# Kernel optimization log

Measured on AMD Instinct MI355X. Metric: run time of the kernel, lower is better.

## Reference

```python
import jax, jax.numpy as jnp
import numpy as np

B, N, C = 8, 4096, 768
H, HD = 12, 64          # num_heads, head_dim = C // H
M = HD * 2              # rand_feat_dim
LAM = 0.3
NUM_STEP = 5


def setup_inputs() -> dict:
    key = jax.random.key(0)
    k1, k2, k3, k4 = jax.random.split(key, 4)
    x = jax.random.normal(k1, (B, N, C), dtype=jnp.float32)
    Wqkv = jax.random.normal(k2, (C, 2 * C), dtype=jnp.float32) * 0.02
    Wproj = jax.random.normal(k3, (C, C), dtype=jnp.float32) * 0.02
    bproj = jnp.zeros((C,), dtype=jnp.float32)
    rand_matrix = jax.random.normal(k4, (H, HD, M), dtype=jnp.float32)
    return {"x": x, "Wqkv": Wqkv, "Wproj": Wproj, "bproj": bproj,
            "rand_matrix": rand_matrix}


def _soft(z, t):
    # sign(z) * relu(|z| - t): soft-thresholding (ISTA proximal step)
    return jnp.sign(z) * jax.nn.relu(jnp.abs(z) - t)


def reference(x, Wqkv, Wproj, bproj, rand_matrix):
    Bn, Nn, Cn = x.shape
    Hh, hd, m = rand_matrix.shape
    scale = hd ** (-0.5)

    qkv = x @ Wqkv                                   # [B,N,2C]
    q = qkv[..., :Cn].reshape(Bn, Nn, Hh, hd).transpose(0, 2, 1, 3)  # [B,H,N,hd]
    v = qkv[..., Cn:].reshape(Bn, Nn, Hh, hd).transpose(0, 2, 1, 3)  # [B,H,N,hd]

    # random-feature map: exp(q @ proj - ||q||^2 / 2) / sqrt(m)
    qs = q * scale ** 0.5
    rf = jnp.exp(jnp.einsum('bhnd,hdm->bhnm', qs, rand_matrix)
                 - 0.5 * jnp.sum(qs * qs, axis=-1, keepdims=True)) / m ** 0.5
    # F.normalize(p=2, dim=-2): normalize over the sequence axis
    qn = rf / jnp.maximum(jnp.linalg.norm(rf, axis=-2, keepdims=True), 1e-12)

    kk = jnp.einsum('bhnm,bhnp->bhmp', qn, qn)       # [B,H,m,m]
    kv = jnp.einsum('bhnm,bhnd->bhmd', qn, v)        # [B,H,m,hd]

    # Lipschitz bound: max row L1 norm of kk, detached
    L = jax.lax.stop_gradient(
        jnp.max(jnp.sum(jnp.abs(kk), axis=-1), axis=-1))[..., None, None] + 1.0

    # unrolled ISTA soft-thresholding loop
    s = _soft(kv, LAM)
    for _ in range(NUM_STEP):
        s = _soft(s - (kk @ s - kv) / L, LAM / L)

    out = jnp.einsum('bhnm,bhmd->bhnd', qn, s)       # [B,H,N,hd]
    out = out.transpose(0, 2, 1, 3).reshape(Bn, Nn, Cn)
    return out @ Wproj + bproj
```

## Files before the change

kernel.cpp:

```cpp
#include <hip/hip_runtime.h>


typedef __attribute__((ext_vector_type(8))) short bf16x8;
typedef __attribute__((ext_vector_type(4))) float f32x4;

#define GLD16(gptr, lptr)                                                              \
  __builtin_amdgcn_global_load_lds((const __attribute__((address_space(1))) void*)(gptr), \
                                   (__attribute__((address_space(3))) void*)(lptr), 16, 0, 0)

__device__ __forceinline__ unsigned short f2bf(float f) {
  union { float f; unsigned int u; } v; v.f = f;
  unsigned int r = v.u + 0x7fffu + ((v.u >> 16) & 1u);
  return (unsigned short)(r >> 16);
}
__device__ __forceinline__ float bf2f(unsigned short s) {
  union { unsigned int u; float f; } v; v.u = ((unsigned int)s) << 16;
  return v.f;
}
__device__ __forceinline__ float rn_of(float css) {
  return 1.f / fmaxf(sqrtf(css), 1e-12f);
}

template<int ITERS>
__device__ __forceinline__ void gemm256_core(
    const unsigned short* __restrict__ A,
    const unsigned short* __restrict__ B,
    int ldk,
    f32x4 (&acc)[8][4],
    unsigned short* smem) {
  const int tid = threadIdx.x;
  const int lane = tid & 63, wave = tid >> 6;
  const int l16 = lane & 15, quad = lane >> 4;
  const int wr = wave >> 2, wc = wave & 3;
  const int rsw = l16 & 7;

#pragma unroll
  for (int i = 0; i < 8; i++)
#pragma unroll
    for (int j = 0; j < 4; j++)
#pragma unroll
      for (int r = 0; r < 4; r++) acc[i][j][r] = 0.f;

  const int srow0 = tid >> 3, sc0 = ((tid & 7) ^ (srow0 & 7)) << 3;
  const int srow1 = (tid + 512) >> 3, sc1 = ((tid & 7) ^ (srow1 & 7)) << 3;
  const int dstw = wave * 512;

  auto stageA = [&](int T, int h) {
    const unsigned short* g = A + (long)(h * 128) * ldk + T * 64;
    unsigned short* d = smem + (T & 1) * 32768 + h * 8192 + dstw;
    GLD16(g + (long)srow0 * ldk + sc0, d);
    GLD16(g + (long)srow1 * ldk + sc1, d + 4096);
  };
  auto stageB = [&](int T, int h) {
    const unsigned short* g = B + (long)(h * 128) * ldk + T * 64;
    unsigned short* d = smem + (T & 1) * 32768 + 16384 + h * 8192 + dstw;
    GLD16(g + (long)srow0 * ldk + sc0, d);
    GLD16(g + (long)srow1 * ldk + sc1, d + 4096);
  };

  bf16x8 af[4][2], bn0[2][2], bn1[2][2];

  auto rdA = [&](int b, int mh) {
    const unsigned short* p = smem + b * 32768 + wr * 8192 + (mh * 64 + l16) * 64;
#pragma unroll
    for (int ii = 0; ii < 4; ii++)
#pragma unroll
      for (int ks = 0; ks < 2; ks++)
        af[ii][ks] = *(const bf16x8*)(p + ii * 1024 + (((ks * 4 + quad) ^ rsw) << 3));
  };
  auto rdB = [&](bf16x8 (&bf)[2][2], int b, int nh) {
    const unsigned short* p = smem + b * 32768 + 16384 + (wc >> 1) * 8192 +
                              ((wc & 1) * 64 + nh * 32 + l16) * 64;
#pragma unroll
    for (int jj = 0; jj < 2; jj++)
#pragma unroll
      for (int ks = 0; ks < 2; ks++)
        bf[jj][ks] = *(const bf16x8*)(p + jj * 1024 + (((ks * 4 + quad) ^ rsw) << 3));
  };

  auto mma = [&](bf16x8 (&bf)[2][2], int mh, int nh) {
    __builtin_amdgcn_s_setprio(1);
#pragma unroll
    for (int ks = 0; ks < 2; ks++)
#pragma unroll
      for (int ii = 0; ii < 4; ii++)
#pragma unroll
        for (int jj = 0; jj < 2; jj++)
          acc[mh * 4 + ii][nh * 2 + jj] = __builtin_amdgcn_mfma_f32_16x16x32_bf16(
              af[ii][ks], bf[jj][ks], acc[mh * 4 + ii][nh * 2 + jj], 0, 0, 0);
    __builtin_amdgcn_s_setprio(0);
  };

#define FENCE asm volatile("" ::: "memory")
#define DRAIN                                             \
  asm volatile("s_waitcnt lgkmcnt(0)" ::: "memory");      \
  __builtin_amdgcn_sched_barrier(0)

  stageA(0, 0); stageA(0, 1); stageB(0, 0); stageB(0, 1);
  stageB(1, 0); stageB(1, 1);
  asm volatile("s_waitcnt vmcnt(4)" ::: "memory");
  __builtin_amdgcn_s_barrier();

#pragma unroll 1
  for (int i = 0; i < ITERS; i++) {
    const int u = 2 * i;
    const bool more = (i < ITERS - 1);
    stageA(u + 1, 0);
    rdA(0, 0); rdB(bn0, 0, 0);
    FENCE; __builtin_amdgcn_s_barrier(); DRAIN;
    mma(bn0, 0, 0);
    FENCE; __builtin_amdgcn_s_barrier();
    stageA(u + 1, 1);
    rdB(bn1, 0, 1);
    FENCE; __builtin_amdgcn_s_barrier(); DRAIN;
    mma(bn1, 0, 1);
    FENCE; __builtin_amdgcn_s_barrier();
    if (more) stageB(u + 2, 0);
    rdA(0, 1);
    FENCE; __builtin_amdgcn_s_barrier(); DRAIN;
    mma(bn1, 1, 1);
    FENCE; __builtin_amdgcn_s_barrier();
    if (more) stageB(u + 2, 1);
    FENCE; __builtin_amdgcn_s_barrier(); DRAIN;
    mma(bn0, 1, 0);
    if (more) { asm volatile("s_waitcnt vmcnt(4)" ::: "memory"); }
    else      { asm volatile("s_waitcnt vmcnt(0)" ::: "memory"); }
    FENCE; __builtin_amdgcn_s_barrier();
    if (more) stageA(u + 2, 0);
    rdA(1, 0); rdB(bn0, 1, 0);
    FENCE; __builtin_amdgcn_s_barrier(); DRAIN;
    mma(bn0, 0, 0);
    FENCE; __builtin_amdgcn_s_barrier();
    if (more) stageA(u + 2, 1);
    rdB(bn1, 1, 1);
    FENCE; __builtin_amdgcn_s_barrier(); DRAIN;
    mma(bn1, 0, 1);
    FENCE; __builtin_amdgcn_s_barrier();
    if (more) stageB(u + 3, 0);
    rdA(1, 1);
    FENCE; __builtin_amdgcn_s_barrier(); DRAIN;
    mma(bn1, 1, 1);
    FENCE; __builtin_amdgcn_s_barrier();
    if (more) stageB(u + 3, 1);
    FENCE; __builtin_amdgcn_s_barrier(); DRAIN;
    mma(bn0, 1, 0);
    asm volatile("s_waitcnt vmcnt(4)" ::: "memory");
    FENCE; __builtin_amdgcn_s_barrier();
  }
#undef FENCE
#undef DRAIN
}

template<int BM, int BN>
__device__ __forceinline__ void gemm_core_nt(
    const unsigned short* __restrict__ A, int lda,
    const unsigned short* __restrict__ B0,
    const unsigned short* __restrict__ B1, int brows0, int ldb,
    int K,
    f32x4 (&acc)[BM / 32][BN / 32],
    unsigned short* As, unsigned short* Bs) {
  constexpr int MT = BM / 32, NT = BN / 32;
  const int tid = threadIdx.x;
  const int lane = tid & 63, wave = tid >> 6;
  const int wm = (wave >> 1) * (BM / 2), wn = (wave & 1) * (BN / 2);
  const int l16 = lane & 15, quad = lane >> 4;
  const int arow = tid >> 2;
  const int akos = (((tid & 3) ^ ((arow >> 1) & 3)) << 3);
  const int fsw = (l16 >> 1) & 3;
#pragma unroll
  for (int i = 0; i < MT; i++)
#pragma unroll
    for (int j = 0; j < NT; j++)
#pragma unroll
      for (int r = 0; r < 4; r++) acc[i][j][r] = 0.f;

  for (int k0 = 0; k0 < K; k0 += 32) {
    __syncthreads();
#pragma unroll
    for (int c = 0; c < BM / 64; c++) {
      const unsigned short* gp = A + (long)(arow + c * 64) * lda + k0 + akos;
      GLD16(gp, As + (c * 256 + wave * 64) * 8);
    }
#pragma unroll
    for (int c = 0; c < BN / 64; c++) {
      int row = arow + c * 64;
      const unsigned short* bp = (row < brows0) ? (B0 + (long)row * ldb)
                                                : (B1 + (long)(row - brows0) * ldb);
      GLD16(bp + k0 + akos, Bs + (c * 256 + wave * 64) * 8);
    }
    __syncthreads();
    bf16x8 af[MT], bfr[NT];
#pragma unroll
    for (int i = 0; i < MT; i++)
      af[i] = *(const bf16x8*)(As + (wm + i * 16 + l16) * 32 + ((quad ^ fsw) * 8));
#pragma unroll
    for (int j = 0; j < NT; j++)
      bfr[j] = *(const bf16x8*)(Bs + (wn + j * 16 + l16) * 32 + ((quad ^ fsw) * 8));
#pragma unroll
    for (int i = 0; i < MT; i++)
#pragma unroll
      for (int j = 0; j < NT; j++)
        acc[i][j] = __builtin_amdgcn_mfma_f32_16x16x32_bf16(af[i], bfr[j], acc[i][j], 0, 0, 0);
  }
}

__global__ __launch_bounds__(256) void k_convert_bf16(const float* __restrict__ in,
                                                      unsigned short* __restrict__ out, long n4) {
  long i = (long)blockIdx.x * 256 + threadIdx.x;
  if (i < n4) {
    float4 v = ((const float4*)in)[i];
    unsigned short o[4] = {f2bf(v.x), f2bf(v.y), f2bf(v.z), f2bf(v.w)};
    ((uint2*)out)[i] = *(uint2*)o;
  }
}

__global__ __launch_bounds__(256) void k_transpose_tiled(const float* __restrict__ in,
                                                         unsigned short* __restrict__ out,
                                                         int R, int C, float scale) {
  __shared__ float t[32][33];
  const float* ib = in + (long)blockIdx.z * R * C;
  unsigned short* ob = out + (long)blockIdx.z * R * C;
  int c0 = blockIdx.x * 32, r0 = blockIdx.y * 32;
  int tx = threadIdx.x & 31, ty = threadIdx.x >> 5;
#pragma unroll
  for (int k = 0; k < 32; k += 8)
    t[ty + k][tx] = ib[(long)(r0 + ty + k) * C + c0 + tx];
  __syncthreads();
#pragma unroll
  for (int k = 0; k < 32; k += 8)
    ob[(long)(c0 + ty + k) * R + r0 + tx] = f2bf(t[tx][ty + k] * scale);
}

__global__ __launch_bounds__(512, 2) void k_gemm_qkv256(const unsigned short* __restrict__ xbf,
                                                        const unsigned short* __restrict__ wqkvT,
                                                        unsigned short* __restrict__ q,
                                                        unsigned short* __restrict__ vT) {
  __shared__ __align__(16) unsigned short smem[65536];
  f32x4 acc[8][4];
  const int L = blockIdx.x;
  const int xcd = L & 7, slot = L >> 3;
  const int rt = xcd * 16 + slot / 6;
  const int ct = slot % 6;
  gemm256_core<6>(xbf + (long)rt * 256 * 768, wqkvT + (long)ct * 256 * 768, 768, acc, smem);

  const int tid = threadIdx.x, lane = tid & 63, wave = tid >> 6;
  const int l16 = lane & 15, quad = lane >> 4;
  const int wr = wave >> 2, wc = wave & 3;
  const int b = rt >> 4;
  const int nbase = (rt & 15) * 256;
  if (ct < 3) {
#pragma unroll
    for (int i = 0; i < 8; i++)
#pragma unroll
      for (int j = 0; j < 4; j++) {
        int col = ct * 256 + wc * 64 + j * 16 + l16;
        int h = col >> 6, d = col & 63;
#pragma unroll
        for (int r = 0; r < 4; r++) {
          int n = nbase + wr * 128 + i * 16 + quad * 4 + r;
          q[((long)(b * 12 + h) * 4096 + n) * 64 + d] = f2bf(acc[i][j][r]);
        }
      }
  } else {
    unsigned short* pool = smem;
    for (int hh = 0; hh < 2; hh++) {
      __syncthreads();
      if (wr == hh) {
#pragma unroll
        for (int i = 0; i < 8; i++)
#pragma unroll
          for (int j = 0; j < 4; j++)
#pragma unroll
            for (int r = 0; r < 4; r++)
              pool[(wc * 64 + j * 16 + l16) * 136 + i * 16 + quad * 4 + r] = f2bf(acc[i][j][r]);
      }
      __syncthreads();
#pragma unroll
      for (int it = 0; it < 8; it++) {
        int chunk = it * 512 + tid;
        int col = chunk >> 4, ng = chunk & 15;
        uint4 val = *(const uint4*)&pool[col * 136 + ng * 8];
        int vcol = (ct - 3) * 256 + col;
        int h = vcol >> 6, d = vcol & 63;
        long n = nbase + hh * 128 + ng * 8;
        *(uint4*)&vT[((long)(b * 12 + h) * 64 + d) * 4096 + n] = val;
      }
    }
  }
}

__global__ __launch_bounds__(256) void k_gemm_rf(const unsigned short* __restrict__ q,
                                                 const unsigned short* __restrict__ rmT,
                                                 unsigned short* __restrict__ qnT,
                                                 float* __restrict__ colss) {
  __shared__ __align__(16) unsigned short smem[16384];
  __shared__ float hnp[256];
  __shared__ float css[128];
  unsigned short* Asm = smem;
  unsigned short* Bsm = smem + 8192;
  unsigned short* pool = smem;
  f32x4 acc[4][4];
  const int nt = blockIdx.x, bh = blockIdx.y, h = bh % 12;
  const int tid = threadIdx.x, lane = tid & 63, wave = tid >> 6;
  const int l16 = lane & 15, quad = lane >> 4;
  const int wm = (wave >> 1) * 64, wn = (wave & 1) * 64;
  const int fsw = (l16 >> 1) & 3;
  const unsigned short* Aq = q + ((long)bh * 4096 + nt * 128) * 64;
  const unsigned short* Brm = rmT + (long)h * 8192;

#pragma unroll
  for (int c = 0; c < 4; c++) {
    int chunk = c * 256 + tid;
    int row = chunk >> 3, ko8 = chunk & 7;
    int kc = ko8 >> 2;
    int c2s = (ko8 & 3) ^ ((row >> 1) & 3);
    *(uint4*)(Asm + kc * 4096 + row * 32 + c2s * 8) = *(const uint4*)(Aq + (long)row * 64 + ko8 * 8);
    *(uint4*)(Bsm + kc * 4096 + row * 32 + c2s * 8) = *(const uint4*)(Brm + (long)row * 64 + ko8 * 8);
  }
  for (int i = tid; i < 128; i += 256) css[i] = 0.f;
  __syncthreads();
  {
    const unsigned short* ap = Asm + (tid & 1) * 4096 + (tid >> 1) * 32;
    float ssum = 0.f;
#pragma unroll
    for (int e = 0; e < 32; e++) { float f = bf2f(ap[e]); ssum += f * f; }
    hnp[tid] = ssum;
  }
#pragma unroll
  for (int i = 0; i < 4; i++)
#pragma unroll
    for (int j = 0; j < 4; j++)
#pragma unroll
      for (int r = 0; r < 4; r++) acc[i][j][r] = 0.f;
#pragma unroll
  for (int kc = 0; kc < 2; kc++) {
    bf16x8 af[4], bfr[4];
#pragma unroll
    for (int i = 0; i < 4; i++)
      af[i] = *(const bf16x8*)(Asm + kc * 4096 + (wm + i * 16 + l16) * 32 + ((quad ^ fsw) * 8));
#pragma unroll
    for (int j = 0; j < 4; j++)
      bfr[j] = *(const bf16x8*)(Bsm + kc * 4096 + (wn + j * 16 + l16) * 32 + ((quad ^ fsw) * 8));
#pragma unroll
    for (int i = 0; i < 4; i++)
#pragma unroll
      for (int j = 0; j < 4; j++)
        acc[i][j] = __builtin_amdgcn_mfma_f32_16x16x32_bf16(af[i], bfr[j], acc[i][j], 0, 0, 0);
  }
  __syncthreads();
  float hnv[4][4];
#pragma unroll
  for (int i = 0; i < 4; i++)
#pragma unroll
    for (int r = 0; r < 4; r++) {
      int row = wm + i * 16 + quad * 4 + r;
      hnv[i][r] = 0.0625f * (hnp[2 * row] + hnp[2 * row + 1]);
    }
#pragma unroll
  for (int j = 0; j < 4; j++) {
    int col = wn + j * 16 + l16;
    float cp = 0.f;
#pragma unroll
    for (int i = 0; i < 4; i++)
#pragma unroll
      for (int r = 0; r < 4; r++) {
        float v = __expf(acc[i][j][r] - hnv[i][r]) * 0.08838834764831845f;
        acc[i][j][r] = v;
        cp += v * v;
      }
    atomicAdd(&css[col], cp);
  }
  __syncthreads();
  for (int i = tid; i < 128; i += 256) atomicAdd(&colss[bh * 128 + i], css[i]);
  for (int hh = 0; hh < 2; hh++) {
    __syncthreads();
    if ((wave >> 1) == hh) {
#pragma unroll
      for (int i = 0; i < 4; i++)
#pragma unroll
        for (int j = 0; j < 4; j++)
#pragma unroll
          for (int r = 0; r < 4; r++)
            pool[(i * 16 + quad * 4 + r) * 134 + wn + j * 16 + l16] = f2bf(acc[i][j][r]);
    }
    __syncthreads();
#pragma unroll
    for (int c = 0; c < 4; c++) {
      int chunk = tid + c * 256;
      int m = chunk >> 3, nj = (chunk & 7) * 8;
      unsigned short o[8];
#pragma unroll
      for (int e = 0; e < 8; e++) o[e] = pool[(nj + e) * 134 + m];
      *(uint4*)&qnT[((long)bh * 128 + m) * 4096 + nt * 128 + hh * 64 + nj] = *(uint4*)o;
    }
  }
}

__global__ __launch_bounds__(256) void k_gemm_kkkv(const unsigned short* __restrict__ qnT,
                                                   const unsigned short* __restrict__ vT,
                                                   const float* __restrict__ colss,
                                                   unsigned short* __restrict__ kkp) {
  __shared__ __align__(16) unsigned short As[128 * 32], Bs[192 * 32];
  f32x4 acc[4][6];
  const int ks = blockIdx.x, bh = blockIdx.y;
  const unsigned short* A = qnT + (long)bh * 128 * 4096 + ks * 512;
  const unsigned short* B1 = vT + (long)bh * 64 * 4096 + ks * 512;
  gemm_core_nt<128, 192>(A, 4096, A, B1, 128, 4096, 512, acc, As, Bs);
  const int lane = threadIdx.x & 63, wave = threadIdx.x >> 6;
  const int l16 = lane & 15, quad = lane >> 4;
  const int wm = (wave >> 1) * 64, wn = (wave & 1) * 96;
  unsigned short* dst = kkp + ((long)ks * 96 + bh) * 24576;
  float rnr[4][4];
#pragma unroll
  for (int i = 0; i < 4; i++)
#pragma unroll
    for (int r = 0; r < 4; r++)
      rnr[i][r] = rn_of(colss[bh * 128 + wm + i * 16 + quad * 4 + r]);
#pragma unroll
  for (int j = 0; j < 6; j++) {
    int col = wn + j * 16 + l16;
    float rnc = (col < 128) ? rn_of(colss[bh * 128 + col]) : 1.f;
#pragma unroll
    for (int i = 0; i < 4; i++)
#pragma unroll
      for (int r = 0; r < 4; r++) {
        int row = wm + i * 16 + quad * 4 + r;
        dst[row * 192 + col] = f2bf(acc[i][j][r] * rnr[i][r] * rnc);
      }
  }
}

__global__ __launch_bounds__(256) void k_ista(const unsigned short* __restrict__ kkp,
                                              const float* __restrict__ colss,
                                              unsigned short* __restrict__ sT) {
  __shared__ __align__(16) unsigned short kks[128 * 144];
  __shared__ __align__(16) unsigned short ssT[64 * 144];
  __shared__ float kvs[128 * 64];
  __shared__ float red[128];
  __shared__ float rns[128];
  const int tid = threadIdx.x, lane = tid & 63, wave = tid >> 6;
  const int l16 = lane & 15, quad = lane >> 4;
  const int wm = (wave >> 1) * 64, wn = (wave & 1) * 32;
  const int bh = blockIdx.x;
  const unsigned short* base = kkp + (long)bh * 24576;
  for (int idx = tid; idx < 3072; idx += 256) {
    int m = idx / 24, c8 = idx % 24;
    float f[8] = {0.f, 0.f, 0.f, 0.f, 0.f, 0.f, 0.f, 0.f};
#pragma unroll
    for (int ks = 0; ks < 8; ks++) {
      union { uint4 u; unsigned short s[8]; } u;
      u.u = *(const uint4*)(base + (long)ks * 2359296 + m * 192 + c8 * 8);
#pragma unroll
      for (int e = 0; e < 8; e++) f[e] += bf2f(u.s[e]);
    }
    if (c8 < 16) {
#pragma unroll
      for (int e = 0; e < 8; e++) kks[m * 144 + c8 * 8 + e] = f2bf(f[e]);
    } else {
#pragma unroll
      for (int e = 0; e < 8; e++) kvs[m * 64 + (c8 - 16) * 8 + e] = f[e];
    }
  }
  __syncthreads();
  float kv[4][2][4];
#pragma unroll
  for (int i = 0; i < 4; i++)
#pragma unroll
    for (int j = 0; j < 2; j++)
#pragma unroll
      for (int r = 0; r < 4; r++) {
        int m = wm + i * 16 + quad * 4 + r, d = wn + j * 16 + l16;
        kv[i][j][r] = kvs[m * 64 + d];
      }
  if (tid < 128) {
    float rs = 0.f;
    const unsigned short* rp = kks + tid * 144;
    for (int p = 0; p < 128; p++) rs += fabsf(bf2f(rp[p]));
    red[tid] = rs;
    rns[tid] = rn_of(colss[bh * 128 + tid]);
  }
  __syncthreads();
  for (int o = 64; o > 0; o >>= 1) {
    if (tid < o) red[tid] = fmaxf(red[tid], red[tid + o]);
    __syncthreads();
  }
  const float L = red[0] + 1.f;
  const float invL = 1.f / L;
  const float lamL = 0.3f * invL;
  float sreg[4][2][4];
#pragma unroll
  for (int i = 0; i < 4; i++)
#pragma unroll
    for (int j = 0; j < 2; j++)
#pragma unroll
      for (int r = 0; r < 4; r++) {
        float z = kv[i][j][r];
        float az = fabsf(z) - 0.3f;
        float s = az > 0.f ? copysignf(az, z) : 0.f;
        sreg[i][j][r] = s;
        ssT[(wn + j * 16 + l16) * 144 + wm + i * 16 + quad * 4 + r] = f2bf(s);
      }
  for (int step = 0; step < 5; step++) {
    __syncthreads();
    f32x4 acc[4][2];
#pragma unroll
    for (int i = 0; i < 4; i++)
#pragma unroll
      for (int j = 0; j < 2; j++)
#pragma unroll
        for (int r = 0; r < 4; r++) acc[i][j][r] = 0.f;
#pragma unroll
    for (int kc = 0; kc < 4; kc++) {
      bf16x8 af[4], bfj[2];
#pragma unroll
      for (int i = 0; i < 4; i++)
        af[i] = *(const bf16x8*)(kks + (wm + i * 16 + l16) * 144 + kc * 32 + quad * 8);
#pragma unroll
      for (int j = 0; j < 2; j++)
        bfj[j] = *(const bf16x8*)(ssT + (wn + j * 16 + l16) * 144 + kc * 32 + quad * 8);
#pragma unroll
      for (int i = 0; i < 4; i++)
#pragma unroll
        for (int j = 0; j < 2; j++)
          acc[i][j] = __builtin_amdgcn_mfma_f32_16x16x32_bf16(af[i], bfj[j], acc[i][j], 0, 0, 0);
    }
    __syncthreads();
#pragma unroll
    for (int i = 0; i < 4; i++)
#pragma unroll
      for (int j = 0; j < 2; j++)
#pragma unroll
        for (int r = 0; r < 4; r++) {
          float z = sreg[i][j][r] - (acc[i][j][r] - kv[i][j][r]) * invL;
          float az = fabsf(z) - lamL;
          float s = az > 0.f ? copysignf(az, z) : 0.f;
          sreg[i][j][r] = s;
          ssT[(wn + j * 16 + l16) * 144 + wm + i * 16 + quad * 4 + r] = f2bf(s);
        }
  }
#pragma unroll
  for (int i = 0; i < 4; i++)
#pragma unroll
    for (int j = 0; j < 2; j++)
#pragma unroll
      for (int r = 0; r < 4; r++) {
        int m = wm + i * 16 + quad * 4 + r, d = wn + j * 16 + l16;
        sT[(long)bh * 8192 + d * 128 + m] = f2bf(sreg[i][j][r] * rns[m]);
      }
}

__global__ __launch_bounds__(256) void k_gemm_attn(const unsigned short* __restrict__ qnT,
                                                   const unsigned short* __restrict__ sT,
                                                   unsigned short* __restrict__ attn) {
  __shared__ __align__(16) unsigned short As2[32 * 128];
  __shared__ __align__(16) unsigned short Bs[64 * 32];
  f32x4 acc[4][2];
  const int nt = blockIdx.x, bh = blockIdx.y;
  const int b = bh / 12, h = bh % 12;
  const int tid = threadIdx.x, lane = tid & 63, wave = tid >> 6;
  const int l16 = lane & 15, quad = lane >> 4;
  const int wm = (wave >> 1) * 64, wn = (wave & 1) * 32;
  const int fsw = (l16 >> 1) & 3;
#pragma unroll
  for (int i = 0; i < 4; i++)
#pragma unroll
    for (int j = 0; j < 2; j++)
#pragma unroll
      for (int r = 0; r < 4; r++) acc[i][j][r] = 0.f;
  for (int k0 = 0; k0 < 128; k0 += 32) {
    __syncthreads();
#pragma unroll
    for (int c = 0; c < 2; c++) {
      int chunk = tid + c * 256;
      int kr = chunk >> 4, n0 = (chunk & 15) * 8;
      const unsigned short* gp = qnT + ((long)bh * 128 + k0 + kr) * 4096 + nt * 128 + n0;
      GLD16(gp, As2 + (c * 256 + wave * 64) * 8);
    }
    {
      int dd = tid >> 2;
      int ko = (((tid & 3) ^ ((dd >> 1) & 3)) * 8);
      const unsigned short* gp = sT + ((long)bh * 64 + dd) * 128 + k0 + ko;
      GLD16(gp, Bs + wave * 512);
    }
    __syncthreads();
    bf16x8 af[4], bfr[2];
#pragma unroll
    for (int i = 0; i < 4; i++) {
      union { bf16x8 v; unsigned short s[8]; } u;
#pragma unroll
      for (int e = 0; e < 8; e++) u.s[e] = As2[(quad * 8 + e) * 128 + wm + i * 16 + l16];
      af[i] = u.v;
    }
#pragma unroll
    for (int j = 0; j < 2; j++)
      bfr[j] = *(const bf16x8*)&Bs[(wn + j * 16 + l16) * 32 + ((quad ^ fsw) * 8)];
#pragma unroll
    for (int i = 0; i < 4; i++)
#pragma unroll
      for (int j = 0; j < 2; j++)
        acc[i][j] = __builtin_amdgcn_mfma_f32_16x16x32_bf16(af[i], bfr[j], acc[i][j], 0, 0, 0);
  }
#pragma unroll
  for (int i = 0; i < 4; i++)
#pragma unroll
    for (int j = 0; j < 2; j++)
#pragma unroll
      for (int r = 0; r < 4; r++) {
        int n = nt * 128 + wm + i * 16 + quad * 4 + r;
        int dd = wn + j * 16 + l16;
        attn[((long)b * 4096 + n) * 768 + h * 64 + dd] = f2bf(acc[i][j][r]);
      }
}

__global__ __launch_bounds__(512, 2) void k_gemm_proj256(const unsigned short* __restrict__ attn,
                                                         const unsigned short* __restrict__ wprojT,
                                                         const float* __restrict__ bias,
                                                         float* __restrict__ out) {
  __shared__ __align__(16) unsigned short smem[65536];
  f32x4 acc[8][4];
  const int L = blockIdx.x;
  const int xcd = L & 7, slot = L >> 3;
  const int rt = xcd * 16 + slot / 3;
  const int ct = slot % 3;
  gemm256_core<6>(attn + (long)rt * 256 * 768, wprojT + (long)ct * 256 * 768, 768, acc, smem);
  const int tid = threadIdx.x, lane = tid & 63, wave = tid >> 6;
  const int l16 = lane & 15, quad = lane >> 4;
  const int wr = wave >> 2, wc = wave & 3;
  const long row0 = (long)rt * 256 + wr * 128;
#pragma unroll
  for (int i = 0; i < 8; i++)
#pragma unroll
    for (int j = 0; j < 4; j++) {
      int col = ct * 256 + wc * 64 + j * 16 + l16;
      float bv = bias[col];
#pragma unroll
      for (int r = 0; r < 4; r++) {
        long row = row0 + i * 16 + quad * 4 + r;
        out[row * 768 + col] = acc[i][j][r] + bv;
      }
    }
}

extern "C" void kernel_launch(void* const* d_in, const int* in_sizes, int n_in,
                              void* d_out, int out_size, void* d_ws, size_t ws_size,
                              hipStream_t stream) {
  const float* x = (const float*)d_in[0];
  const float* Wqkv = (const float*)d_in[1];
  const float* Wproj = (const float*)d_in[2];
  const float* bproj = (const float*)d_in[3];
  const float* rm = (const float*)d_in[4];
  float* out = (float*)d_out;

  size_t o = 0;
  char* wsb = (char*)d_ws;
  auto take = [&](size_t b) { char* p = wsb + o; o += b; return p; };
  unsigned short* wqkvT = (unsigned short*)take(2359296);
  unsigned short* wprojT = (unsigned short*)take(1179648);
  unsigned short* rmT = (unsigned short*)take(196608);
  unsigned short* q = (unsigned short*)take(50331648);
  unsigned short* vT = (unsigned short*)take(50331648);
  float* colss = (float*)take(49152);
  unsigned short* sT = (unsigned short*)take(1572864);
  if (ws_size < o) return;

  unsigned short* xbf = (unsigned short*)d_out;
  unsigned short* qnT = (unsigned short*)d_out;
  unsigned short* kkp = q;
  unsigned short* attnbf = q;

  hipMemsetAsync(colss, 0, 49152, stream);

  k_convert_bf16<<<24576, 256, 0, stream>>>(x, xbf, 6291456L);
  k_transpose_tiled<<<dim3(48, 24, 1), 256, 0, stream>>>(Wqkv, wqkvT, 768, 1536, 1.0f);
  k_transpose_tiled<<<dim3(24, 24, 1), 256, 0, stream>>>(Wproj, wprojT, 768, 768, 1.0f);
  k_transpose_tiled<<<dim3(4, 2, 12), 256, 0, stream>>>(rm, rmT, 64, 128, 0.3535533905932738f);
  k_gemm_qkv256<<<768, 512, 0, stream>>>(xbf, wqkvT, q, vT);
  k_gemm_rf<<<dim3(32, 96), 256, 0, stream>>>(q, rmT, qnT, colss);
  k_gemm_kkkv<<<dim3(8, 96), 256, 0, stream>>>(qnT, vT, colss, kkp);
  k_ista<<<96, 256, 0, stream>>>(kkp, colss, sT);
  k_gemm_attn<<<dim3(32, 96), 256, 0, stream>>>(qnT, sT, attnbf);
  k_gemm_proj256<<<384, 512, 0, stream>>>(attnbf, wprojT, bproj, out);
}
```

Measured before the change: 452.4 us.

## Restructure 256-tile GEMM main loop into K-split phases with partial LDS waits

Reorganizes the 256x256 GEMM inner loop from eight quarter-tile phases into four phases. Each phase loads the B fragments for all four N columns and computes a full 4x4 MFMA block per K-substep. LDS reads are split by K-substep, with partial lgkmcnt waits so the first MFMA batch can start while the second half's fragments are still arriving. Global staging is regrouped accordingly with a vmcnt(2) wait. This halves the number of barriers per iteration and overlaps LDS latency with compute, at the cost of holding more B fragments in registers and a more delicate wait-count schedule.

```diff
diff --git a/kernel.cpp b/kernel.cpp
--- a/kernel.cpp
+++ b/kernel.cpp
@@ -58,43 +58,36 @@
     GLD16(g + (long)srow1 * ldk + sc1, d + 4096);
   };
 
-  bf16x8 af[4][2], bn0[2][2], bn1[2][2];
-
-  auto rdA = [&](int b, int mh) {
+  bf16x8 af[4][2], bn[4][2];
+
+  auto rdA_ks = [&](int b, int mh, int ks) {
     const unsigned short* p = smem + b * 32768 + wr * 8192 + (mh * 64 + l16) * 64;
 #pragma unroll
     for (int ii = 0; ii < 4; ii++)
-#pragma unroll
-      for (int ks = 0; ks < 2; ks++)
-        af[ii][ks] = *(const bf16x8*)(p + ii * 1024 + (((ks * 4 + quad) ^ rsw) << 3));
+      af[ii][ks] = *(const bf16x8*)(p + ii * 1024 + (((ks * 4 + quad) ^ rsw) << 3));
   };
-  auto rdB = [&](bf16x8 (&bf)[2][2], int b, int nh) {
+  auto rdB_ks = [&](int b, int ks) {
     const unsigned short* p = smem + b * 32768 + 16384 + (wc >> 1) * 8192 +
-                              ((wc & 1) * 64 + nh * 32 + l16) * 64;
-#pragma unroll
-    for (int jj = 0; jj < 2; jj++)
-#pragma unroll
-      for (int ks = 0; ks < 2; ks++)
-        bf[jj][ks] = *(const bf16x8*)(p + jj * 1024 + (((ks * 4 + quad) ^ rsw) << 3));
+                              ((wc & 1) * 64 + l16) * 64;
+#pragma unroll
+    for (int jj = 0; jj < 4; jj++)
+      bn[jj][ks] = *(const bf16x8*)(p + jj * 1024 + (((ks * 4 + quad) ^ rsw) << 3));
   };
 
-  auto mma = [&](bf16x8 (&bf)[2][2], int mh, int nh) {
+  auto mma16 = [&](int mh, int ks) {
     __builtin_amdgcn_s_setprio(1);
 #pragma unroll
-    for (int ks = 0; ks < 2; ks++)
-#pragma unroll
-      for (int ii = 0; ii < 4; ii++)
-#pragma unroll
-        for (int jj = 0; jj < 2; jj++)
-          acc[mh * 4 + ii][nh * 2 + jj] = __builtin_amdgcn_mfma_f32_16x16x32_bf16(
-              af[ii][ks], bf[jj][ks], acc[mh * 4 + ii][nh * 2 + jj], 0, 0, 0);
+    for (int ii = 0; ii < 4; ii++)
+#pragma unroll
+      for (int jj = 0; jj < 4; jj++)
+        acc[mh * 4 + ii][jj] = __builtin_amdgcn_mfma_f32_16x16x32_bf16(
+            af[ii][ks], bn[jj][ks], acc[mh * 4 + ii][jj], 0, 0, 0);
     __builtin_amdgcn_s_setprio(0);
   };
 
 #define FENCE asm volatile("" ::: "memory")
-#define DRAIN                                             \
-  asm volatile("s_waitcnt lgkmcnt(0)" ::: "memory");      \
-  __builtin_amdgcn_sched_barrier(0)
+#define SGB __builtin_amdgcn_sched_barrier(0)
+#define LGKM(n) asm volatile("s_waitcnt lgkmcnt(" #n ")" ::: "memory")
 
   stageA(0, 0); stageA(0, 1); stageB(0, 0); stageB(0, 1);
   stageB(1, 0); stageB(1, 1);
@@ -104,51 +97,55 @@
 #pragma unroll 1
   for (int i = 0; i < ITERS; i++) {
     const int u = 2 * i;
-    const bool more = (i < ITERS - 1);
+    const bool more = (i + 1 < ITERS);
     stageA(u + 1, 0);
-    rdA(0, 0); rdB(bn0, 0, 0);
-    FENCE; __builtin_amdgcn_s_barrier(); DRAIN;
-    mma(bn0, 0, 0);
+    rdB_ks(0, 0); rdA_ks(0, 0, 0);
+    SGB;
+    rdB_ks(0, 1); rdA_ks(0, 0, 1);
+    FENCE; __builtin_amdgcn_s_barrier();
+    LGKM(8); SGB;
+    mma16(0, 0);
+    LGKM(0); SGB;
+    mma16(0, 1);
     FENCE; __builtin_amdgcn_s_barrier();
     stageA(u + 1, 1);
-    rdB(bn1, 0, 1);
-    FENCE; __builtin_amdgcn_s_barrier(); DRAIN;
-    mma(bn1, 0, 1);
-    FENCE; __builtin_amdgcn_s_barrier();
     if (more) stageB(u + 2, 0);
-    rdA(0, 1);
-    FENCE; __builtin_amdgcn_s_barrier(); DRAIN;
-    mma(bn1, 1, 1);
-    FENCE; __builtin_amdgcn_s_barrier();
-    if (more) stageB(u + 2, 1);
-    FENCE; __builtin_amdgcn_s_barrier(); DRAIN;
-    mma(bn0, 1, 0);
+    rdA_ks(0, 1, 0);
+    SGB;
+    rdA_ks(0, 1, 1);
+    FENCE; __builtin_amdgcn_s_barrier();
+    LGKM(4); SGB;
+    mma16(1, 0);
+    LGKM(0); SGB;
+    mma16(1, 1);
+    if (more) { asm volatile("s_waitcnt vmcnt(2)" ::: "memory"); }
+    else      { asm volatile("s_waitcnt vmcnt(0)" ::: "memory"); }
+    FENCE; __builtin_amdgcn_s_barrier();
+    if (more) { stageB(u + 2, 1); stageA(u + 2, 0); stageA(u + 2, 1); }
+    rdB_ks(1, 0); rdA_ks(1, 0, 0);
+    SGB;
+    rdB_ks(1, 1); rdA_ks(1, 0, 1);
+    FENCE; __builtin_amdgcn_s_barrier();
+    LGKM(8); SGB;
+    mma16(0, 0);
+    LGKM(0); SGB;
+    mma16(0, 1);
+    FENCE; __builtin_amdgcn_s_barrier();
+    if (more) { stageB(u + 3, 0); stageB(u + 3, 1); }
+    rdA_ks(1, 1, 0);
+    SGB;
+    rdA_ks(1, 1, 1);
+    FENCE; __builtin_amdgcn_s_barrier();
+    LGKM(4); SGB;
+    mma16(1, 0);
+    LGKM(0); SGB;
+    mma16(1, 1);
     if (more) { asm volatile("s_waitcnt vmcnt(4)" ::: "memory"); }
-    else      { asm volatile("s_waitcnt vmcnt(0)" ::: "memory"); }
-    FENCE; __builtin_amdgcn_s_barrier();
-    if (more) stageA(u + 2, 0);
-    rdA(1, 0); rdB(bn0, 1, 0);
-    FENCE; __builtin_amdgcn_s_barrier(); DRAIN;
-    mma(bn0, 0, 0);
-    FENCE; __builtin_amdgcn_s_barrier();
-    if (more) stageA(u + 2, 1);
-    rdB(bn1, 1, 1);
-    FENCE; __builtin_amdgcn_s_barrier(); DRAIN;
-    mma(bn1, 0, 1);
-    FENCE; __builtin_amdgcn_s_barrier();
-    if (more) stageB(u + 3, 0);
-    rdA(1, 1);
-    FENCE; __builtin_amdgcn_s_barrier(); DRAIN;
-    mma(bn1, 1, 1);
-    FENCE; __builtin_amdgcn_s_barrier();
-    if (more) stageB(u + 3, 1);
-    FENCE; __builtin_amdgcn_s_barrier(); DRAIN;
-    mma(bn0, 1, 0);
-    asm volatile("s_waitcnt vmcnt(4)" ::: "memory");
     FENCE; __builtin_amdgcn_s_barrier();
   }
 #undef FENCE
-#undef DRAIN
+#undef SGB
+#undef LGKM
 }
 
 template<int BM, int BN>
```

Result: no change. 455.0 us (+0.6%).
